# Optimization experiments

Hardware: AMD Instinct MI355X
Metric: run time of the kernel (lower is better)

Reference implementation:

```python
import jax, jax.numpy as jnp
import numpy as np

N_NODES = 65536
IN_DIM = 512
OUT_DIM = 512
N_EDGES = 524288
BN_EPS = 1e-5
NORM_EPS = 1e-6


def setup_inputs() -> dict:
    key = jax.random.key(0)
    k1, k2, k3, k4 = jax.random.split(key, 4)
    features = jax.random.normal(k1, (N_NODES, IN_DIM), dtype=jnp.float32)
    edge_index = jax.random.randint(k2, (2, N_EDGES), 0, N_NODES, dtype=jnp.int64)
    # torch Linear weight layout: [out_features, in_features] with in = 2*IN_DIM
    W = jax.random.normal(k3, (OUT_DIM, 2 * IN_DIM), dtype=jnp.float32) * (1.0 / np.sqrt(2 * IN_DIM))
    b = jax.random.normal(k4, (OUT_DIM,), dtype=jnp.float32) * 0.01
    gamma = jnp.ones((OUT_DIM,), dtype=jnp.float32)
    beta = jnp.zeros((OUT_DIM,), dtype=jnp.float32)
    running_mean = jnp.zeros((OUT_DIM,), dtype=jnp.float32)
    running_var = jnp.ones((OUT_DIM,), dtype=jnp.float32)
    return {
        "features": features,
        "edge_index": edge_index,
        "W": W,
        "b": b,
        "gamma": gamma,
        "beta": beta,
        "running_mean": running_mean,
        "running_var": running_var,
    }


def reference(features, edge_index, W, b, gamma, beta, running_mean, running_var):
    sources = edge_index[0]
    targets = edge_index[1]
    # scatter-sum of neighbor (target) features into source rows  [N, D]
    aggregated = jax.ops.segment_sum(features[targets], sources, num_segments=N_NODES)
    out = jnp.concatenate([features, aggregated], axis=1)  # [N, 2D]
    out = out @ W.T + b  # [N, OUT_DIM]
    out = jax.nn.relu(out)
    # BatchNorm1d (eval mode, running stats)
    out = (out - running_mean) * jax.lax.rsqrt(running_var + BN_EPS) * gamma + beta
    # dropout is identity in inference
    out = out / (jnp.linalg.norm(out, axis=1, keepdims=True) + NORM_EPS)
    return out
```

## Files before the change

### kernel.cpp

```cpp
#include <hip/hip_runtime.h>
#include <hip/hip_bf16.h>

#define N_NODES 65536
#define DIM 512
#define N_EDGES 524288
#define BN_EPS 1e-5f
#define NORM_EPS 1e-6f
#define CAP 32

typedef __attribute__((ext_vector_type(8))) short short8;
typedef __attribute__((ext_vector_type(4))) float f32x4;

static __device__ __forceinline__ unsigned f2bf(float f) {
    union { float f; unsigned u; } c; c.f = f;
    unsigned u = c.u;
    return (u + 0x7fffu + ((u >> 16) & 1u)) >> 16;
}
static __device__ __forceinline__ float bf16lo(unsigned u) {
    union { unsigned u; float f; } c; c.u = u << 16; return c.f;
}
static __device__ __forceinline__ float bf16hi(unsigned u) {
    union { unsigned u; float f; } c; c.u = u & 0xffff0000u; return c.f;
}
static __device__ __forceinline__ uint4 pack8(float4 a, float4 b) {
    uint4 o;
    o.x = f2bf(a.x) | (f2bf(a.y) << 16);
    o.y = f2bf(a.z) | (f2bf(a.w) << 16);
    o.z = f2bf(b.x) | (f2bf(b.y) << 16);
    o.w = f2bf(b.z) | (f2bf(b.w) << 16);
    return o;
}

#define NB_SCAT  2048
#define NB_CONVF 16384
#define NB_CONVW 256

__global__ void megaprep_kernel(const float* __restrict__ features,
                                unsigned short* __restrict__ Xb,
                                const float* __restrict__ W,
                                unsigned short* __restrict__ Wb,
                                const int* __restrict__ src,
                                const int* __restrict__ tgt,
                                int* __restrict__ counts,
                                unsigned short* __restrict__ bucket) {
    int b = blockIdx.x;
    if (b < NB_SCAT) {
        int e = b * 256 + threadIdx.x;
        int s = src[e];
        int pos = atomicAdd(&counts[s], 1);
        if (pos < CAP) bucket[s * CAP + pos] = (unsigned short)tgt[e];
    } else if (b < NB_SCAT + NB_CONVF) {
        int i = (b - NB_SCAT) * 256 + threadIdx.x;
        const float4* s = (const float4*)features + i * 2;
        ((uint4*)Xb)[i] = pack8(s[0], s[1]);
    } else {
        int i = (b - NB_SCAT - NB_CONVF) * 256 + threadIdx.x;
        const float4* s = (const float4*)W + i * 2;
        ((uint4*)Wb)[i] = pack8(s[0], s[1]);
    }
}

static __device__ __forceinline__ void acc8(float* a, uint4 v) {
    a[0] += bf16lo(v.x); a[1] += bf16hi(v.x);
    a[2] += bf16lo(v.y); a[3] += bf16hi(v.y);
    a[4] += bf16lo(v.z); a[5] += bf16hi(v.z);
    a[6] += bf16lo(v.w); a[7] += bf16hi(v.w);
}

__global__ void aggregate_kernel(const unsigned short* __restrict__ Xb,
                                 const int* __restrict__ counts,
                                 const unsigned short* __restrict__ bucket,
                                 unsigned short* __restrict__ agg) {
    int wave = (blockIdx.x * blockDim.x + threadIdx.x) >> 6;
    int lane = threadIdx.x & 63;
    if (wave >= N_NODES) return;
    int deg = counts[wave];
    if (deg > CAP) deg = CAP;
    const unsigned short* brow = bucket + wave * CAP;
    float a[8] = {0.f, 0.f, 0.f, 0.f, 0.f, 0.f, 0.f, 0.f};
    float b[8] = {0.f, 0.f, 0.f, 0.f, 0.f, 0.f, 0.f, 0.f};
    const uint4* F = (const uint4*)Xb;
    int i = 0;
    for (; i + 8 <= deg; i += 8) {
        int t0 = brow[i],     t1 = brow[i + 1], t2 = brow[i + 2], t3 = brow[i + 3];
        int t4 = brow[i + 4], t5 = brow[i + 5], t6 = brow[i + 6], t7 = brow[i + 7];
        uint4 v0 = F[t0 * 64 + lane];
        uint4 v1 = F[t1 * 64 + lane];
        uint4 v2 = F[t2 * 64 + lane];
        uint4 v3 = F[t3 * 64 + lane];
        uint4 v4 = F[t4 * 64 + lane];
        uint4 v5 = F[t5 * 64 + lane];
        uint4 v6 = F[t6 * 64 + lane];
        uint4 v7 = F[t7 * 64 + lane];
        acc8(a, v0); acc8(b, v1); acc8(a, v2); acc8(b, v3);
        acc8(a, v4); acc8(b, v5); acc8(a, v6); acc8(b, v7);
    }
    for (; i + 4 <= deg; i += 4) {
        int t0 = brow[i], t1 = brow[i + 1], t2 = brow[i + 2], t3 = brow[i + 3];
        uint4 v0 = F[t0 * 64 + lane];
        uint4 v1 = F[t1 * 64 + lane];
        uint4 v2 = F[t2 * 64 + lane];
        uint4 v3 = F[t3 * 64 + lane];
        acc8(a, v0); acc8(b, v1); acc8(a, v2); acc8(b, v3);
    }
    for (; i < deg; ++i) {
        int t0 = brow[i];
        uint4 v0 = F[t0 * 64 + lane];
        acc8(a, v0);
    }
#pragma unroll
    for (int k = 0; k < 8; ++k) a[k] += b[k];
    uint4 o;
    o.x = f2bf(a[0]) | (f2bf(a[1]) << 16);
    o.y = f2bf(a[2]) | (f2bf(a[3]) << 16);
    o.z = f2bf(a[4]) | (f2bf(a[5]) << 16);
    o.w = f2bf(a[6]) | (f2bf(a[7]) << 16);
    ((uint4*)agg)[wave * 64 + lane] = o;
}

__global__ __launch_bounds__(512, 4) void fused_gemm_norm_kernel(
        const unsigned short* __restrict__ Xb,
        const unsigned short* __restrict__ agg,
        const unsigned short* __restrict__ Wb,
        const float* __restrict__ bias,
        const float* __restrict__ gamma,
        const float* __restrict__ beta,
        const float* __restrict__ rmean,
        const float* __restrict__ rvar,
        float* __restrict__ out) {
    __shared__ uint4 Alds[512];
    __shared__ uint4 Blds[4096];
    __shared__ float ssm[64][8];

    const int t = threadIdx.x;
    const int m0 = blockIdx.x * 64;
    const int w = t >> 6, L = t & 63;
    const int ml = L & 15, quad = L >> 4;
    const int wn = w * 64;

    float bi[4], sc[4], sh[4];
#pragma unroll
    for (int ni = 0; ni < 4; ++ni) {
        int col = wn + ni * 16 + ml;
        bi[ni] = bias[col];
        sc[ni] = gamma[col] * __frsqrt_rn(rvar[col] + BN_EPS);
        sh[ni] = beta[col] - rmean[col] * sc[ni];
    }

    f32x4 acc[4][4];
#pragma unroll
    for (int mi = 0; mi < 4; ++mi)
#pragma unroll
        for (int ni = 0; ni < 4; ++ni)
            acc[mi][ni] = (f32x4){0.f, 0.f, 0.f, 0.f};

    for (int kt = 0; kt < 16; ++kt) {
        const unsigned short* Asrc = (kt < 8) ? (Xb + kt * 64) : (agg + (kt - 8) * 64);
        __syncthreads();
        {
            int r = t >> 3, pp = t & 7;
            int p = pp ^ (r & 7);
            const unsigned short* ga = Asrc + (m0 + r) * 512 + p * 8;
            char* la = (char*)Alds + (t & 448) * 16;
            __builtin_amdgcn_global_load_lds(
                (const __attribute__((address_space(1))) unsigned int*)ga,
                (__attribute__((address_space(3))) unsigned int*)la, 16, 0, 0);
        }
#pragma unroll
        for (int j = 0; j < 8; ++j) {
            int c = j * 512 + t;
            int r = c >> 3, pp = c & 7;
            int p = pp ^ (r & 7);
            const unsigned short* gb = Wb + r * 1024 + kt * 64 + p * 8;
            char* lb = (char*)Blds + (j * 512 + (t & 448)) * 16;
            __builtin_amdgcn_global_load_lds(
                (const __attribute__((address_space(1))) unsigned int*)gb,
                (__attribute__((address_space(3))) unsigned int*)lb, 16, 0, 0);
        }
        __syncthreads();
#pragma unroll
        for (int kc = 0; kc < 2; ++kc) {
            int g = kc * 4 + quad;
            short8 a[4], b[4];
#pragma unroll
            for (int mi = 0; mi < 4; ++mi) {
                int ra = mi * 16 + ml;
                a[mi] = *(const short8*)&Alds[ra * 8 + (g ^ (ra & 7))];
                int rb = wn + mi * 16 + ml;
                b[mi] = *(const short8*)&Blds[rb * 8 + (g ^ (rb & 7))];
            }
#pragma unroll
            for (int mi = 0; mi < 4; ++mi)
#pragma unroll
                for (int ni = 0; ni < 4; ++ni)
                    acc[mi][ni] = __builtin_amdgcn_mfma_f32_16x16x32_bf16(
                        a[mi], b[ni], acc[mi][ni], 0, 0, 0);
        }
    }

    float ss[4][4];
#pragma unroll
    for (int mi = 0; mi < 4; ++mi)
#pragma unroll
        for (int r = 0; r < 4; ++r)
            ss[mi][r] = 0.f;
#pragma unroll
    for (int mi = 0; mi < 4; ++mi)
#pragma unroll
        for (int ni = 0; ni < 4; ++ni)
#pragma unroll
            for (int r = 0; r < 4; ++r) {
                float v = fmaxf(acc[mi][ni][r] + bi[ni], 0.f) * sc[ni] + sh[ni];
                acc[mi][ni][r] = v;
                ss[mi][r] += v * v;
            }
#pragma unroll
    for (int mi = 0; mi < 4; ++mi)
#pragma unroll
        for (int r = 0; r < 4; ++r) {
#pragma unroll
            for (int d = 1; d < 16; d <<= 1)
                ss[mi][r] += __shfl_xor(ss[mi][r], d);
        }
    if (ml == 0) {
#pragma unroll
        for (int mi = 0; mi < 4; ++mi)
#pragma unroll
            for (int r = 0; r < 4; ++r)
                ssm[mi * 16 + quad * 4 + r][w] = ss[mi][r];
    }
    __syncthreads();
#pragma unroll
    for (int mi = 0; mi < 4; ++mi)
#pragma unroll
        for (int r = 0; r < 4; ++r) {
            int rl = mi * 16 + quad * 4 + r;
            const float4* sp = (const float4*)ssm[rl];
            float4 s0 = sp[0], s1 = sp[1];
            float tot = s0.x + s0.y + s0.z + s0.w + s1.x + s1.y + s1.z + s1.w;
            float inv = 1.f / (sqrtf(tot) + NORM_EPS);
            int m = m0 + rl;
#pragma unroll
            for (int ni = 0; ni < 4; ++ni)
                out[m * 512 + wn + ni * 16 + ml] = acc[mi][ni][r] * inv;
        }
}

extern "C" void kernel_launch(void* const* d_in, const int* in_sizes, int n_in,
                              void* d_out, int out_size, void* d_ws, size_t ws_size,
                              hipStream_t stream) {
    const float* features = (const float*)d_in[0];
    const int* edges      = (const int*)d_in[1];
    const float* W        = (const float*)d_in[2];
    const float* bias     = (const float*)d_in[3];
    const float* gamma    = (const float*)d_in[4];
    const float* beta     = (const float*)d_in[5];
    const float* rmean    = (const float*)d_in[6];
    const float* rvar     = (const float*)d_in[7];
    float* out = (float*)d_out;

    char* ws = (char*)d_ws;
    int* counts            = (int*)(ws);
    unsigned short* bucket = (unsigned short*)(ws + 0x100000);
    unsigned short* Wb     = (unsigned short*)(ws + 0x500000);
    unsigned short* Xb     = (unsigned short*)(ws + 0x600000);
    unsigned short* agg    = (unsigned short*)(ws + 0x4600000);

    const int* src = edges;
    const int* tgt = edges + N_EDGES;

    hipMemsetAsync(counts, 0, N_NODES * sizeof(int), stream);
    megaprep_kernel<<<NB_SCAT + NB_CONVF + NB_CONVW, 256, 0, stream>>>(
        features, Xb, W, Wb, src, tgt, counts, bucket);
    aggregate_kernel<<<N_NODES / 4, 256, 0, stream>>>(Xb, counts, bucket, agg);
    fused_gemm_norm_kernel<<<N_NODES / 64, 512, 0, stream>>>(
        Xb, agg, Wb, bias, gamma, beta, rmean, rvar, out);
}
```

Before: 412.6 us.

## Fuse neighbor aggregation into the GEMM kernel prologue

Removes the separate aggregate kernel launch. Each GEMM block first gathers and sums the neighbor features for its own 64 rows, one wave handling 8 nodes, writes them to the agg buffer, waits on its memory ops and syncs before the GEMM reads them. This saves one launch and lets the fresh agg rows be reused from cache, but the latency-bound gather now runs serially inside the GEMM blocks with less memory-level parallelism and the register pressure of the GEMM kernel. Cross-wave visibility of agg relies on the global writes being seen after the barrier.

```diff
diff --git a/kernel.cpp b/kernel.cpp
--- a/kernel.cpp
+++ b/kernel.cpp
@@ -67,61 +67,12 @@
     a[6] += bf16lo(v.w); a[7] += bf16hi(v.w);
 }
 
-__global__ void aggregate_kernel(const unsigned short* __restrict__ Xb,
-                                 const int* __restrict__ counts,
-                                 const unsigned short* __restrict__ bucket,
-                                 unsigned short* __restrict__ agg) {
-    int wave = (blockIdx.x * blockDim.x + threadIdx.x) >> 6;
-    int lane = threadIdx.x & 63;
-    if (wave >= N_NODES) return;
-    int deg = counts[wave];
-    if (deg > CAP) deg = CAP;
-    const unsigned short* brow = bucket + wave * CAP;
-    float a[8] = {0.f, 0.f, 0.f, 0.f, 0.f, 0.f, 0.f, 0.f};
-    float b[8] = {0.f, 0.f, 0.f, 0.f, 0.f, 0.f, 0.f, 0.f};
-    const uint4* F = (const uint4*)Xb;
-    int i = 0;
-    for (; i + 8 <= deg; i += 8) {
-        int t0 = brow[i],     t1 = brow[i + 1], t2 = brow[i + 2], t3 = brow[i + 3];
-        int t4 = brow[i + 4], t5 = brow[i + 5], t6 = brow[i + 6], t7 = brow[i + 7];
-        uint4 v0 = F[t0 * 64 + lane];
-        uint4 v1 = F[t1 * 64 + lane];
-        uint4 v2 = F[t2 * 64 + lane];
-        uint4 v3 = F[t3 * 64 + lane];
-        uint4 v4 = F[t4 * 64 + lane];
-        uint4 v5 = F[t5 * 64 + lane];
-        uint4 v6 = F[t6 * 64 + lane];
-        uint4 v7 = F[t7 * 64 + lane];
-        acc8(a, v0); acc8(b, v1); acc8(a, v2); acc8(b, v3);
-        acc8(a, v4); acc8(b, v5); acc8(a, v6); acc8(b, v7);
-    }
-    for (; i + 4 <= deg; i += 4) {
-        int t0 = brow[i], t1 = brow[i + 1], t2 = brow[i + 2], t3 = brow[i + 3];
-        uint4 v0 = F[t0 * 64 + lane];
-        uint4 v1 = F[t1 * 64 + lane];
-        uint4 v2 = F[t2 * 64 + lane];
-        uint4 v3 = F[t3 * 64 + lane];
-        acc8(a, v0); acc8(b, v1); acc8(a, v2); acc8(b, v3);
-    }
-    for (; i < deg; ++i) {
-        int t0 = brow[i];
-        uint4 v0 = F[t0 * 64 + lane];
-        acc8(a, v0);
-    }
-#pragma unroll
-    for (int k = 0; k < 8; ++k) a[k] += b[k];
-    uint4 o;
-    o.x = f2bf(a[0]) | (f2bf(a[1]) << 16);
-    o.y = f2bf(a[2]) | (f2bf(a[3]) << 16);
-    o.z = f2bf(a[4]) | (f2bf(a[5]) << 16);
-    o.w = f2bf(a[6]) | (f2bf(a[7]) << 16);
-    ((uint4*)agg)[wave * 64 + lane] = o;
-}
-
 __global__ __launch_bounds__(512, 4) void fused_gemm_norm_kernel(
         const unsigned short* __restrict__ Xb,
-        const unsigned short* __restrict__ agg,
+        unsigned short* __restrict__ agg,
         const unsigned short* __restrict__ Wb,
+        const int* __restrict__ counts,
+        const unsigned short* __restrict__ bucket,
         const float* __restrict__ bias,
         const float* __restrict__ gamma,
         const float* __restrict__ beta,
@@ -137,6 +88,50 @@
     const int w = t >> 6, L = t & 63;
     const int ml = L & 15, quad = L >> 4;
     const int wn = w * 64;
+
+    {
+        const uint4* F = (const uint4*)Xb;
+        uint4* AGQ = (uint4*)agg;
+        for (int rr = 0; rr < 8; ++rr) {
+            int node = m0 + w * 8 + rr;
+            int deg = counts[node];
+            if (deg > CAP) deg = CAP;
+            const unsigned short* brow = bucket + node * CAP;
+            float a[8] = {0.f, 0.f, 0.f, 0.f, 0.f, 0.f, 0.f, 0.f};
+            float b[8] = {0.f, 0.f, 0.f, 0.f, 0.f, 0.f, 0.f, 0.f};
+            int i = 0;
+            for (; i + 4 <= deg; i += 4) {
+                int t0 = brow[i], t1 = brow[i + 1], t2 = brow[i + 2], t3 = brow[i + 3];
+                uint4 v0 = F[t0 * 64 + L];
+                uint4 v1 = F[t1 * 64 + L];
+                uint4 v2 = F[t2 * 64 + L];
+                uint4 v3 = F[t3 * 64 + L];
+                acc8(a, v0); acc8(b, v1); acc8(a, v2); acc8(b, v3);
+            }
+            if (i + 2 <= deg) {
+                int t0 = brow[i], t1 = brow[i + 1];
+                uint4 v0 = F[t0 * 64 + L];
+                uint4 v1 = F[t1 * 64 + L];
+                acc8(a, v0); acc8(b, v1);
+                i += 2;
+            }
+            if (i < deg) {
+                int t0 = brow[i];
+                uint4 v0 = F[t0 * 64 + L];
+                acc8(a, v0);
+            }
+#pragma unroll
+            for (int k = 0; k < 8; ++k) a[k] += b[k];
+            uint4 o;
+            o.x = f2bf(a[0]) | (f2bf(a[1]) << 16);
+            o.y = f2bf(a[2]) | (f2bf(a[3]) << 16);
+            o.z = f2bf(a[4]) | (f2bf(a[5]) << 16);
+            o.w = f2bf(a[6]) | (f2bf(a[7]) << 16);
+            AGQ[node * 64 + L] = o;
+        }
+        asm volatile("s_waitcnt vmcnt(0)" ::: "memory");
+    }
+    __syncthreads();
 
     float bi[4], sc[4], sh[4];
 #pragma unroll
@@ -272,7 +267,6 @@
     hipMemsetAsync(counts, 0, N_NODES * sizeof(int), stream);
     megaprep_kernel<<<NB_SCAT + NB_CONVF + NB_CONVW, 256, 0, stream>>>(
         features, Xb, W, Wb, src, tgt, counts, bucket);
-    aggregate_kernel<<<N_NODES / 4, 256, 0, stream>>>(Xb, counts, bucket, agg);
     fused_gemm_norm_kernel<<<N_NODES / 64, 512, 0, stream>>>(
-        Xb, agg, Wb, bias, gamma, beta, rmean, rvar, out);
-}
+        Xb, agg, Wb, counts, bucket, bias, gamma, beta, rmean, rvar, out);
+}
```

Result: slower. 423.3 us (+2.6%).
